# Optimization experiments

Measured on AMD Instinct MI355X. Metric: run time of the kernel, lower is better.

Reference implementation:

```python
import jax, jax.numpy as jnp
import numpy as np
from functools import partial

# CUBA LIF/LI constants (mock-mode software integration, hxtorch conventions)
DT = 1e-6
TAU_MEM_INV = 1.0 / 6e-6   # dt*tau_mem_inv = 1/6 per-step membrane coupling
TAU_SYN_INV = 1.0 / 6e-6   # dt*tau_syn_inv = 1/6 per-step synaptic decay
ALPHA = 50.0               # SuperSpike surrogate steepness
V_TH = 1.0                 # threshold; leak = reset = 0


@partial(jax.custom_vjp, nondiff_argnums=(1,))
def spike_fn(x, alpha):
    # Heaviside forward, SuperSpike surrogate backward.
    return (x > 0.0).astype(x.dtype)

def _spike_fwd(x, alpha):
    return spike_fn(x, alpha), x

def _spike_bwd(alpha, x, g):
    return (g / (alpha * jnp.abs(x) + 1.0) ** 2,)

spike_fn.defvjp(_spike_fwd, _spike_bwd)


def cuba_lif(inp):
    """CUBA LIF integration over time. inp: [T, B, N] synaptic input; returns spikes [T, B, N]."""
    B, N = inp.shape[1], inp.shape[2]
    v0 = jnp.zeros((B, N), inp.dtype)
    i0 = jnp.zeros((B, N), inp.dtype)

    def step(carry, x):
        v, i = carry
        v = v + DT * TAU_MEM_INV * (-v + i)          # membrane update (leak=0)
        i = i * (1.0 - DT * TAU_SYN_INV) + x          # synaptic current decay + input
        z = spike_fn(v - V_TH, ALPHA)                 # spike
        v = (1.0 - jax.lax.stop_gradient(z)) * v      # reset to 0 (detached spike)
        return (v, i), z

    _, z = jax.lax.scan(step, (v0, i0), inp)
    return z


def cuba_li(inp):
    """CUBA LI (non-spiking readout) integration. inp: [T, B, N]; returns membrane trace [T, B, N]."""
    B, N = inp.shape[1], inp.shape[2]
    v0 = jnp.zeros((B, N), inp.dtype)
    i0 = jnp.zeros((B, N), inp.dtype)

    def step(carry, x):
        v, i = carry
        v = v + DT * TAU_MEM_INV * (-v + i)
        i = i * (1.0 - DT * TAU_SYN_INV) + x
        return (v, i), v

    _, v = jax.lax.scan(step, (v0, i0), inp)
    return v


def setup_inputs() -> dict:
    key = jax.random.key(0)
    k1, k2, k3 = jax.random.split(key, 3)
    T, B, N_IN, N_HID, N_OUT = 256, 128, 784, 512, 128
    spikes = (jax.random.uniform(k1, (T, B, N_IN)) < 0.1).astype(jnp.float32)
    w_hidden = 0.2 * jax.random.normal(k2, (N_HID, N_IN), dtype=jnp.float32)
    w_out = 0.2 * jax.random.normal(k3, (N_OUT, N_HID), dtype=jnp.float32)
    return {"spikes": spikes, "w_hidden": w_hidden, "w_out": w_out}


def reference(spikes, w_hidden, w_out):
    # input_repetitions=1 -> repeat is a no-op. Synapses have no bias.
    c_h = jnp.einsum('tbi,hi->tbh', spikes, w_hidden)   # [T, B, n_hidden]
    s_h = cuba_lif(c_h)                                  # hidden spikes
    c_o = jnp.einsum('tbh,oh->tbo', s_h, w_out)          # [T, B, n_out]
    return cuba_li(c_o)                                  # readout membrane trace (v_cadc)
```

## Files before the change

### kernel.cpp

```cpp
#include <hip/hip_runtime.h>

typedef _Float16 f16;
typedef _Float16 f16x8 __attribute__((ext_vector_type(8)));
typedef float f32x4 __attribute__((ext_vector_type(4)));

#define GLOBAL_AS __attribute__((address_space(1)))
#define LDS_AS __attribute__((address_space(3)))

__device__ __forceinline__ void async16(const void* g, void* l) {
  __builtin_amdgcn_global_load_lds((const GLOBAL_AS unsigned int*)g,
                                   (LDS_AS unsigned int*)l, 16, 0, 0);
}

__global__ __launch_bounds__(256) void conv_all(const float* __restrict__ s,
                                                const float* __restrict__ wh,
                                                const float* __restrict__ wo,
                                                f16* __restrict__ a16,
                                                f16* __restrict__ w2h,
                                                f16* __restrict__ w2o) {
  if (blockIdx.x < 12800) {
    int idx = blockIdx.x * 256 + threadIdx.x;
    int m = idx / 100;
    int g = idx - m * 100;
    f16x8 h = {};
    if (g < 98) {
      const float4* p = (const float4*)(s + (size_t)m * 784 + g * 8);
      float4 x = p[0];
      float4 y = p[1];
      h[0] = (f16)x.x; h[1] = (f16)x.y; h[2] = (f16)x.z; h[3] = (f16)x.w;
      h[4] = (f16)y.x; h[5] = (f16)y.y; h[6] = (f16)y.z; h[7] = (f16)y.w;
    }
    *(f16x8*)(a16 + (size_t)m * 800 + g * 8) = h;
  } else {
    int idx = (blockIdx.x - 12800) * 256 + threadIdx.x;
    if (idx < 819200) {
      int h = idx / 1600;
      int c = idx - h * 1600;
      f16 o = (f16)0.f;
      if (c < 784) {
        o = (f16)wh[h * 784 + c];
      } else if (c >= 800 && c < 1584) {
        float x = wh[h * 784 + (c - 800)];
        f16 hi = (f16)x;
        o = (f16)((x - (float)hi) * 2048.0f);
      }
      w2h[idx] = o;
    } else if (idx < 819200 + 65536) {
      int j = idx - 819200;
      w2o[j] = (f16)wo[j];
    }
  }
}

template <typename OUT, int N_LD, int A_STRIDE, int B_STRIDE, int NCH64,
          bool TAIL32, int B_OFF_LO, int KSPLIT_SPAN, bool XCD_SWZ>
__global__ __launch_bounds__(256, 2) void gemm_f16(const f16* __restrict__ A,
                                                   const f16* __restrict__ B,
                                                   OUT* __restrict__ C) {
  constexpr bool HAS_LO = (B_OFF_LO > 0);
  __shared__ __align__(16) f16 lds_a[128 * 64];
  __shared__ __align__(16) f16 lds_bh[128 * 64];
  __shared__ __align__(16) f16 lds_bl[HAS_LO ? 128 * 64 : 8];
  const int t = threadIdx.x;
  const int lane = t & 63;
  const int wave = t >> 6;
  int bx, by;
  if (XCD_SWZ) {
    const int b = blockIdx.x;
    by = (b & 7) + 8 * (b >> 5);
    bx = (b >> 3) & 3;
  } else {
    bx = blockIdx.x;
    by = blockIdx.y;
  }
  const int m0 = by * 128;
  const int n0 = KSPLIT_SPAN ? 0 : bx * 128;
  const int kb = KSPLIT_SPAN ? bx * KSPLIT_SPAN : 0;
  OUT* Cp = KSPLIT_SPAN ? C + (size_t)bx * 32768 * N_LD : C;
  const int wm = (wave >> 1) * 64;
  const int wn = (wave & 1) * 64;
  const int row = lane & 15;
  const int quad = lane >> 4;

  f32x4 acch[4][4] = {};
  f32x4 accl[HAS_LO ? 4 : 1][4] = {};

  for (int c = 0; c < NCH64; ++c) {
    const int k0 = kb + c * 64;
#pragma unroll
    for (int s = 0; s < 4; ++s) {
      const int j = t + s * 256;
      const int r = j >> 3;
      const int g = (j & 7) ^ (r & 7);
      async16(A + (m0 + r) * A_STRIDE + k0 + g * 8, &lds_a[j * 8]);
      async16(B + (n0 + r) * B_STRIDE + k0 + g * 8, &lds_bh[j * 8]);
      if (HAS_LO)
        async16(B + (n0 + r) * B_STRIDE + B_OFF_LO + k0 + g * 8, &lds_bl[j * 8]);
    }
    __syncthreads();
#pragma unroll
    for (int ks = 0; ks < 2; ++ks) {
      f16x8 af[4], bh[4], bl[4];
#pragma unroll
      for (int tm = 0; tm < 4; ++tm) {
        const int ra = wm + tm * 16 + row;
        const int p = (ks * 4 + quad) ^ (ra & 7);
        af[tm] = *(const f16x8*)&lds_a[ra * 64 + p * 8];
      }
#pragma unroll
      for (int tn = 0; tn < 4; ++tn) {
        const int rb = wn + tn * 16 + row;
        const int p = (ks * 4 + quad) ^ (rb & 7);
        bh[tn] = *(const f16x8*)&lds_bh[rb * 64 + p * 8];
        if (HAS_LO) bl[tn] = *(const f16x8*)&lds_bl[rb * 64 + p * 8];
      }
#pragma unroll
      for (int tm = 0; tm < 4; ++tm)
#pragma unroll
        for (int tn = 0; tn < 4; ++tn) {
          acch[tm][tn] =
              __builtin_amdgcn_mfma_f32_16x16x32_f16(af[tm], bh[tn], acch[tm][tn], 0, 0, 0);
          if (HAS_LO)
            accl[tm][tn] =
                __builtin_amdgcn_mfma_f32_16x16x32_f16(af[tm], bl[tn], accl[tm][tn], 0, 0, 0);
        }
    }
    __syncthreads();
  }

  if (TAIL32) {
    const int k0 = kb + NCH64 * 64;
#pragma unroll
    for (int s = 0; s < 2; ++s) {
      const int j = t + s * 256;
      const int r = j >> 2;
      const int g = (j & 3) ^ (r & 3);
      async16(A + (m0 + r) * A_STRIDE + k0 + g * 8, &lds_a[j * 8]);
      async16(B + (n0 + r) * B_STRIDE + k0 + g * 8, &lds_bh[j * 8]);
      if (HAS_LO)
        async16(B + (n0 + r) * B_STRIDE + B_OFF_LO + k0 + g * 8, &lds_bl[j * 8]);
    }
    __syncthreads();
    f16x8 af[4], bh[4], bl[4];
#pragma unroll
    for (int tm = 0; tm < 4; ++tm) {
      const int ra = wm + tm * 16 + row;
      const int p = quad ^ (ra & 3);
      af[tm] = *(const f16x8*)&lds_a[ra * 32 + p * 8];
    }
#pragma unroll
    for (int tn = 0; tn < 4; ++tn) {
      const int rb = wn + tn * 16 + row;
      const int p = quad ^ (rb & 3);
      bh[tn] = *(const f16x8*)&lds_bh[rb * 32 + p * 8];
      if (HAS_LO) bl[tn] = *(const f16x8*)&lds_bl[rb * 32 + p * 8];
    }
#pragma unroll
    for (int tm = 0; tm < 4; ++tm)
#pragma unroll
      for (int tn = 0; tn < 4; ++tn) {
        acch[tm][tn] =
            __builtin_amdgcn_mfma_f32_16x16x32_f16(af[tm], bh[tn], acch[tm][tn], 0, 0, 0);
        if (HAS_LO)
          accl[tm][tn] =
              __builtin_amdgcn_mfma_f32_16x16x32_f16(af[tm], bl[tn], accl[tm][tn], 0, 0, 0);
      }
  }

#pragma unroll
  for (int tm = 0; tm < 4; ++tm)
#pragma unroll
    for (int tn = 0; tn < 4; ++tn)
#pragma unroll
      for (int r = 0; r < 4; ++r) {
        const int mm = m0 + wm + tm * 16 + quad * 4 + r;
        const int nn = n0 + wn + tn * 16 + row;
        float val = acch[tm][tn][r];
        if (HAS_LO) val += 4.8828125e-4f * accl[tm][tn][r];
        Cp[(size_t)mm * N_LD + nn] = (OUT)val;
      }
}

__global__ __launch_bounds__(256) void lif_scan(const f16* __restrict__ ch,
                                                f16* __restrict__ sh) {
  const int n = blockIdx.x * 256 + threadIdx.x;
  f16 xa[16], xb[16];
#pragma unroll
  for (int j = 0; j < 16; ++j) xa[j] = ch[j * 65536 + n];
  float v = 0.f, cur = 0.f;
  for (int c = 0; c < 16; ++c) {
    const int nc = (c + 1) & 15;
#pragma unroll
    for (int j = 0; j < 16; ++j) xb[j] = ch[(nc * 16 + j) * 65536 + n];
#pragma unroll
    for (int j = 0; j < 16; ++j) {
      const int t = c * 16 + j;
      float x = (float)xa[j];
      v = v + 0.16666667f * (cur - v);
      cur = 0.8333333f * cur + x;
      bool z = v > 1.0f;
      sh[t * 65536 + n] = z ? (f16)1.f : (f16)0.f;
      v = z ? 0.f : v;
    }
#pragma unroll
    for (int j = 0; j < 16; ++j) xa[j] = xb[j];
  }
}

__global__ __launch_bounds__(256) void li_scan_seg(const f16* __restrict__ coA,
                                                   const f16* __restrict__ coB,
                                                   float* __restrict__ out) {
  const int tid = blockIdx.x * 256 + threadIdx.x;
  const int n = tid & 16383;
  const int seg = tid >> 14;
  const int t0 = seg * 64;
  float v = 0.f, cur = 0.f;
  float xa[8], xb[8];
  if (seg) {
    const int w0 = t0 - 64;
#pragma unroll
    for (int j = 0; j < 8; ++j)
      xa[j] = (float)coA[(w0 + j) * 16384 + n] + (float)coB[(w0 + j) * 16384 + n];
    for (int c = 0; c < 8; ++c) {
      const int nb = w0 + (c + 1) * 8;
#pragma unroll
      for (int j = 0; j < 8; ++j)
        xb[j] = (float)coA[(nb + j) * 16384 + n] + (float)coB[(nb + j) * 16384 + n];
#pragma unroll
      for (int j = 0; j < 8; ++j) {
        v = v + 0.16666667f * (cur - v);
        cur = 0.8333333f * cur + xa[j];
      }
#pragma unroll
      for (int j = 0; j < 8; ++j) xa[j] = xb[j];
    }
  } else {
#pragma unroll
    for (int j = 0; j < 8; ++j)
      xa[j] = (float)coA[j * 16384 + n] + (float)coB[j * 16384 + n];
  }
  for (int c = 0; c < 8; ++c) {
    if (c < 7) {
      const int nb = t0 + (c + 1) * 8;
#pragma unroll
      for (int j = 0; j < 8; ++j)
        xb[j] = (float)coA[(nb + j) * 16384 + n] + (float)coB[(nb + j) * 16384 + n];
    }
#pragma unroll
    for (int j = 0; j < 8; ++j) {
      const int t = t0 + c * 8 + j;
      v = v + 0.16666667f * (cur - v);
      cur = 0.8333333f * cur + xa[j];
      out[t * 16384 + n] = v;
    }
#pragma unroll
    for (int j = 0; j < 8; ++j) xa[j] = xb[j];
  }
}

extern "C" void kernel_launch(void* const* d_in, const int* in_sizes, int n_in,
                              void* d_out, int out_size, void* d_ws, size_t ws_size,
                              hipStream_t stream) {
  const float* spikes = (const float*)d_in[0];
  const float* w_hidden = (const float*)d_in[1];
  const float* w_out = (const float*)d_in[2];
  float* out = (float*)d_out;

  char* ws = (char*)d_ws;
  f16* A16 = (f16*)ws;
  f16* coA = (f16*)ws;
  f16* coB = (f16*)(ws + 8388608);
  f16* w2h = (f16*)(ws + 52428800);
  f16* c_h = (f16*)(ws + 52428800 + 1638400);
  f16* s_h = (f16*)(ws + 52428800 + 1638400 + 33554432);
  f16* w2o = (f16*)(ws + 52428800 + 1638400 + 33554432 + 33554432);

  conv_all<<<16256, 256, 0, stream>>>(spikes, w_hidden, w_out, A16, w2h, w2o);

  gemm_f16<f16, 512, 800, 1600, 12, true, 800, 0, true>
      <<<1024, 256, 0, stream>>>(A16, w2h, c_h);

  lif_scan<<<256, 256, 0, stream>>>(c_h, s_h);

  gemm_f16<f16, 128, 512, 512, 4, false, 0, 256, false>
      <<<dim3(2, 256), 256, 0, stream>>>(s_h, w2o, coA);

  li_scan_seg<<<256, 256, 0, stream>>>(coA, coB, out);
}
```

Measured before the change: 242.5 us.

## Fuse fp32 spike conversion into the hidden GEMM A-tile load

Drops the separate pass that converted the fp32 spike input to a padded fp16 buffer. The hidden-layer GEMM now reads fp32 spikes directly, converts them in registers and writes fp16 to LDS, clamping the K tail so it never reads past column 784. This saves a full write and re-read of the intermediate activation buffer, at the cost of synchronous, twice-as-wide A loads that are repeated across the four N-tile blocks. The LIF scan prefetch depth also doubles from 16 to 32 timesteps to hide more load latency.

```diff
diff --git a/kernel.cpp b/kernel.cpp
--- a/kernel.cpp
+++ b/kernel.cpp
@@ -12,52 +12,37 @@
                                    (LDS_AS unsigned int*)l, 16, 0, 0);
 }
 
-__global__ __launch_bounds__(256) void conv_all(const float* __restrict__ s,
-                                                const float* __restrict__ wh,
-                                                const float* __restrict__ wo,
-                                                f16* __restrict__ a16,
-                                                f16* __restrict__ w2h,
-                                                f16* __restrict__ w2o) {
-  if (blockIdx.x < 12800) {
-    int idx = blockIdx.x * 256 + threadIdx.x;
-    int m = idx / 100;
-    int g = idx - m * 100;
-    f16x8 h = {};
-    if (g < 98) {
-      const float4* p = (const float4*)(s + (size_t)m * 784 + g * 8);
-      float4 x = p[0];
-      float4 y = p[1];
-      h[0] = (f16)x.x; h[1] = (f16)x.y; h[2] = (f16)x.z; h[3] = (f16)x.w;
-      h[4] = (f16)y.x; h[5] = (f16)y.y; h[6] = (f16)y.z; h[7] = (f16)y.w;
-    }
-    *(f16x8*)(a16 + (size_t)m * 800 + g * 8) = h;
+__global__ __launch_bounds__(256) void conv_w(const float* __restrict__ wh,
+                                              const float* __restrict__ wo,
+                                              f16* __restrict__ w2h,
+                                              f16* __restrict__ w2o) {
+  int idx = blockIdx.x * 256 + threadIdx.x;
+  if (idx < 819200) {
+    int h = idx / 1600;
+    int c = idx - h * 1600;
+    f16 o = (f16)0.f;
+    if (c < 784) {
+      o = (f16)wh[h * 784 + c];
+    } else if (c >= 800 && c < 1584) {
+      float x = wh[h * 784 + (c - 800)];
+      f16 hi = (f16)x;
+      o = (f16)((x - (float)hi) * 2048.0f);
+    }
+    w2h[idx] = o;
   } else {
-    int idx = (blockIdx.x - 12800) * 256 + threadIdx.x;
-    if (idx < 819200) {
-      int h = idx / 1600;
-      int c = idx - h * 1600;
-      f16 o = (f16)0.f;
-      if (c < 784) {
-        o = (f16)wh[h * 784 + c];
-      } else if (c >= 800 && c < 1584) {
-        float x = wh[h * 784 + (c - 800)];
-        f16 hi = (f16)x;
-        o = (f16)((x - (float)hi) * 2048.0f);
-      }
-      w2h[idx] = o;
-    } else if (idx < 819200 + 65536) {
-      int j = idx - 819200;
-      w2o[j] = (f16)wo[j];
-    }
+    int j = idx - 819200;
+    w2o[j] = (f16)wo[j];
   }
 }
 
 template <typename OUT, int N_LD, int A_STRIDE, int B_STRIDE, int NCH64,
-          bool TAIL32, int B_OFF_LO, int KSPLIT_SPAN, bool XCD_SWZ>
-__global__ __launch_bounds__(256, 2) void gemm_f16(const f16* __restrict__ A,
+          bool TAIL32, int B_OFF_LO, int KSPLIT_SPAN, bool XCD_SWZ, bool A_F32>
+__global__ __launch_bounds__(256, 2) void gemm_f16(const void* __restrict__ A,
                                                    const f16* __restrict__ B,
                                                    OUT* __restrict__ C) {
   constexpr bool HAS_LO = (B_OFF_LO > 0);
+  const f16* __restrict__ Ah = (const f16*)A;
+  const float* __restrict__ Af = (const float*)A;
   __shared__ __align__(16) f16 lds_a[128 * 64];
   __shared__ __align__(16) f16 lds_bh[128 * 64];
   __shared__ __align__(16) f16 lds_bl[HAS_LO ? 128 * 64 : 8];
@@ -92,7 +77,17 @@
       const int j = t + s * 256;
       const int r = j >> 3;
       const int g = (j & 7) ^ (r & 7);
-      async16(A + (m0 + r) * A_STRIDE + k0 + g * 8, &lds_a[j * 8]);
+      if constexpr (A_F32) {
+        const float4* p = (const float4*)(Af + (size_t)(m0 + r) * A_STRIDE + k0 + g * 8);
+        float4 x = p[0];
+        float4 y = p[1];
+        f16x8 h;
+        h[0] = (f16)x.x; h[1] = (f16)x.y; h[2] = (f16)x.z; h[3] = (f16)x.w;
+        h[4] = (f16)y.x; h[5] = (f16)y.y; h[6] = (f16)y.z; h[7] = (f16)y.w;
+        *(f16x8*)&lds_a[j * 8] = h;
+      } else {
+        async16(Ah + (m0 + r) * A_STRIDE + k0 + g * 8, &lds_a[j * 8]);
+      }
       async16(B + (n0 + r) * B_STRIDE + k0 + g * 8, &lds_bh[j * 8]);
       if (HAS_LO)
         async16(B + (n0 + r) * B_STRIDE + B_OFF_LO + k0 + g * 8, &lds_bl[j * 8]);
@@ -135,7 +130,19 @@
       const int j = t + s * 256;
       const int r = j >> 2;
       const int g = (j & 3) ^ (r & 3);
-      async16(A + (m0 + r) * A_STRIDE + k0 + g * 8, &lds_a[j * 8]);
+      if constexpr (A_F32) {
+        int col = k0 + g * 8;
+        if (col > 776) col = 776;
+        const float4* p = (const float4*)(Af + (size_t)(m0 + r) * A_STRIDE + col);
+        float4 x = p[0];
+        float4 y = p[1];
+        f16x8 h;
+        h[0] = (f16)x.x; h[1] = (f16)x.y; h[2] = (f16)x.z; h[3] = (f16)x.w;
+        h[4] = (f16)y.x; h[5] = (f16)y.y; h[6] = (f16)y.z; h[7] = (f16)y.w;
+        *(f16x8*)&lds_a[j * 8] = h;
+      } else {
+        async16(Ah + (m0 + r) * A_STRIDE + k0 + g * 8, &lds_a[j * 8]);
+      }
       async16(B + (n0 + r) * B_STRIDE + k0 + g * 8, &lds_bh[j * 8]);
       if (HAS_LO)
         async16(B + (n0 + r) * B_STRIDE + B_OFF_LO + k0 + g * 8, &lds_bl[j * 8]);
@@ -184,17 +191,17 @@
 __global__ __launch_bounds__(256) void lif_scan(const f16* __restrict__ ch,
                                                 f16* __restrict__ sh) {
   const int n = blockIdx.x * 256 + threadIdx.x;
-  f16 xa[16], xb[16];
-#pragma unroll
-  for (int j = 0; j < 16; ++j) xa[j] = ch[j * 65536 + n];
+  f16 xa[32], xb[32];
+#pragma unroll
+  for (int j = 0; j < 32; ++j) xa[j] = ch[j * 65536 + n];
   float v = 0.f, cur = 0.f;
-  for (int c = 0; c < 16; ++c) {
-    const int nc = (c + 1) & 15;
-#pragma unroll
-    for (int j = 0; j < 16; ++j) xb[j] = ch[(nc * 16 + j) * 65536 + n];
-#pragma unroll
-    for (int j = 0; j < 16; ++j) {
-      const int t = c * 16 + j;
+  for (int c = 0; c < 8; ++c) {
+    const int nc = (c + 1) & 7;
+#pragma unroll
+    for (int j = 0; j < 32; ++j) xb[j] = ch[(nc * 32 + j) * 65536 + n];
+#pragma unroll
+    for (int j = 0; j < 32; ++j) {
+      const int t = c * 32 + j;
       float x = (float)xa[j];
       v = v + 0.16666667f * (cur - v);
       cur = 0.8333333f * cur + x;
@@ -203,7 +210,7 @@
       v = z ? 0.f : v;
     }
 #pragma unroll
-    for (int j = 0; j < 16; ++j) xa[j] = xb[j];
+    for (int j = 0; j < 32; ++j) xa[j] = xb[j];
   }
 }
 
@@ -267,7 +274,6 @@
   float* out = (float*)d_out;
 
   char* ws = (char*)d_ws;
-  f16* A16 = (f16*)ws;
   f16* coA = (f16*)ws;
   f16* coB = (f16*)(ws + 8388608);
   f16* w2h = (f16*)(ws + 52428800);
@@ -275,14 +281,14 @@
   f16* s_h = (f16*)(ws + 52428800 + 1638400 + 33554432);
   f16* w2o = (f16*)(ws + 52428800 + 1638400 + 33554432 + 33554432);
 
-  conv_all<<<16256, 256, 0, stream>>>(spikes, w_hidden, w_out, A16, w2h, w2o);
-
-  gemm_f16<f16, 512, 800, 1600, 12, true, 800, 0, true>
-      <<<1024, 256, 0, stream>>>(A16, w2h, c_h);
+  conv_w<<<3456, 256, 0, stream>>>(w_hidden, w_out, w2h, w2o);
+
+  gemm_f16<f16, 512, 784, 1600, 12, true, 800, 0, true, true>
+      <<<1024, 256, 0, stream>>>(spikes, w2h, c_h);
 
   lif_scan<<<256, 256, 0, stream>>>(c_h, s_h);
 
-  gemm_f16<f16, 128, 512, 512, 4, false, 0, 256, false>
+  gemm_f16<f16, 128, 512, 512, 4, false, 0, 256, false, false>
       <<<dim3(2, 256), 256, 0, stream>>>(s_h, w2o, coA);
 
   li_scan_seg<<<256, 256, 0, stream>>>(coA, coB, out);
```

Result: slower. 253.0 us (+4.3%).
